# Performance work log

Measured on AMD Instinct MI355X. Metric: run time of the kernel, lower is better.

## Reference

```python
import jax, jax.numpy as jnp
import numpy as np

B, C, H, W = 2, 512, 64, 64
G = 32  # GroupNorm groups
EPS = 1e-6


def setup_inputs() -> dict:
    key = jax.random.key(0)
    ks = jax.random.split(key, 6)
    s = 1.0 / np.sqrt(C)
    return {
        "x": jax.random.normal(ks[0], (B, C, H, W), dtype=jnp.float32),
        "gn_w": jnp.ones((C,), dtype=jnp.float32),
        "gn_b": jnp.zeros((C,), dtype=jnp.float32),
        "wq": jax.random.normal(ks[1], (C, C), dtype=jnp.float32) * s,
        "bq": jnp.zeros((C,), dtype=jnp.float32),
        "wk": jax.random.normal(ks[2], (C, C), dtype=jnp.float32) * s,
        "bk": jnp.zeros((C,), dtype=jnp.float32),
        "wv": jax.random.normal(ks[3], (C, C), dtype=jnp.float32) * s,
        "bv": jnp.zeros((C,), dtype=jnp.float32),
        "wo": jax.random.normal(ks[4], (C, C), dtype=jnp.float32) * s,
        "bo": jnp.zeros((C,), dtype=jnp.float32),
    }


def _group_norm(x, w, b):
    b_, c_, h_, w_ = x.shape
    xg = x.reshape(b_, G, c_ // G, h_ * w_)
    mu = jnp.mean(xg, axis=(2, 3), keepdims=True)
    var = jnp.var(xg, axis=(2, 3), keepdims=True)
    xn = (xg - mu) * jax.lax.rsqrt(var + EPS)
    xn = xn.reshape(b_, c_, h_ * w_)
    return xn * w[None, :, None] + b[None, :, None]  # [B, C, N]


def reference(x, gn_w, gn_b, wq, bq, wk, bk, wv, bv, wo, bo):
    b, c, h, w = x.shape
    hn = _group_norm(x, gn_w, gn_b)  # [B, C, N]
    # 1x1 convs == per-pixel matmuls over channel dim
    q = jnp.einsum('oc,bcn->bon', wq, hn) + bq[None, :, None]
    k = jnp.einsum('oc,bcn->bon', wk, hn) + bk[None, :, None]
    v = jnp.einsum('oc,bcn->bon', wv, hn) + bv[None, :, None]
    scale = jnp.asarray(c, x.dtype) ** -0.5
    attn = jnp.einsum('bci,bcj->bij', q, k) * scale  # [B, N, N]
    attn = jax.nn.softmax(attn, axis=-1)
    o = jnp.einsum('bij,bcj->bci', attn, v)  # [B, C, N]
    o = jnp.einsum('oc,bcn->bon', wo, o) + bo[None, :, None]
    return x + o.reshape(b, c, h, w)
```

## Files before the change

### kernel.cpp

```cpp
#include <hip/hip_runtime.h>

#define CC 512
#define NPIX 4096
#define NB 2
#define NG 32
#define GSIZE 16
#define EPS 1e-6f

typedef unsigned short u16;
typedef __bf16 bf16x8 __attribute__((ext_vector_type(8)));
typedef float f32x4 __attribute__((ext_vector_type(4)));

__device__ __forceinline__ float bf2f(u16 u) {
  union { unsigned int i; float f; } c; c.i = ((unsigned int)u) << 16; return c.f;
}
__device__ __forceinline__ u16 f2bf(float f) {
  union { float f; unsigned int i; } c; c.f = f;
  unsigned int u = c.i;
  return (u16)((u + 0x7fffu + ((u >> 16) & 1u)) >> 16);
}

__global__ __launch_bounds__(256) void f2bf4x4_kernel(
    const float* __restrict__ s0, const float* __restrict__ s1,
    const float* __restrict__ s2, const float* __restrict__ s3,
    u16* __restrict__ d0, u16* __restrict__ d1,
    u16* __restrict__ d2, u16* __restrict__ d3) {
  const float* s; u16* d;
  switch (blockIdx.y) {
    case 0: s = s0; d = d0; break;
    case 1: s = s1; d = d1; break;
    case 2: s = s2; d = d2; break;
    default: s = s3; d = d3; break;
  }
  int i = blockIdx.x * 256 + threadIdx.x;
  float4 v = ((const float4*)s)[i];
  uint2 pk;
  pk.x = (unsigned)f2bf(v.x) | ((unsigned)f2bf(v.y) << 16);
  pk.y = (unsigned)f2bf(v.z) | ((unsigned)f2bf(v.w) << 16);
  ((uint2*)d)[i] = pk;
}

__global__ __launch_bounds__(256) void concat2_kernel(const float* __restrict__ a,
                                                      const float* __restrict__ b,
                                                      float* __restrict__ o) {
  int i = blockIdx.x * 256 + threadIdx.x;
  o[i] = (i < CC) ? a[i] : b[i - CC];
}

__global__ __launch_bounds__(256) void gn_stats_kernel(const float* __restrict__ x,
                                                       float* __restrict__ stats) {
  int bg = blockIdx.x;
  const float4* p = (const float4*)(x + (long)bg * (GSIZE * NPIX));
  float s = 0.f, ss = 0.f;
  for (int i = threadIdx.x; i < GSIZE * NPIX / 4; i += 256) {
    float4 v = p[i];
    s  += v.x + v.y + v.z + v.w;
    ss += v.x * v.x + v.y * v.y + v.z * v.z + v.w * v.w;
  }
  for (int off = 32; off; off >>= 1) { s += __shfl_xor(s, off); ss += __shfl_xor(ss, off); }
  __shared__ float rs[4], rss[4];
  int wid = threadIdx.x >> 6;
  if ((threadIdx.x & 63) == 0) { rs[wid] = s; rss[wid] = ss; }
  __syncthreads();
  if (threadIdx.x == 0) {
    s = rs[0] + rs[1] + rs[2] + rs[3];
    ss = rss[0] + rss[1] + rss[2] + rss[3];
    float mean = s / (float)(GSIZE * NPIX);
    float var = ss / (float)(GSIZE * NPIX) - mean * mean;
    stats[bg * 2] = mean;
    stats[bg * 2 + 1] = rsqrtf(var + EPS);
  }
}

__global__ __launch_bounds__(256) void gn_apply_kernel(const float* __restrict__ x,
                                                       const float* __restrict__ stats,
                                                       const float* __restrict__ gw,
                                                       const float* __restrict__ gb,
                                                       u16* __restrict__ hn) {
  int n0 = blockIdx.x * 64, c0 = blockIdx.y * 64, b = blockIdx.z;
  __shared__ float tile[64][65];
  int t = threadIdx.x;
  int nj = t & 63, cw = t >> 6;
  #pragma unroll
  for (int r = 0; r < 16; ++r) {
    int ci = cw * 16 + r;
    int c = c0 + ci;
    float mean = stats[(b * NG + (c >> 4)) * 2];
    float rstd = stats[(b * NG + (c >> 4)) * 2 + 1];
    float v = x[((long)b * CC + c) * NPIX + n0 + nj];
    tile[ci][nj] = (v - mean) * rstd * gw[c] + gb[c];
  }
  __syncthreads();
  #pragma unroll
  for (int r = 0; r < 16; ++r) {
    int nn = cw * 16 + r;
    hn[((long)b * NPIX + n0 + nn) * CC + c0 + nj] = f2bf(tile[nj][nn]);
  }
}

#define BM 128
#define BN 128
#define BKT 64
#define BUFSZ 8192

template<int OUTF32, int BIASMODE, int RESID>
__global__ __launch_bounds__(256) void gemm_nt(
    const u16* __restrict__ A, int lda, long aBatch,
    const u16* __restrict__ B, int ldb, long bBatch,
    void* __restrict__ C, int ldc, long cBatch,
    const float* __restrict__ bias,
    const float* __restrict__ resid, long rBatch,
    int K, float scale) {
  __shared__ u16 SH[2 * 2 * BUFSZ];
  const int t = threadIdx.x;

  int nwgx = gridDim.x, nwgy = gridDim.y;
  int flat = blockIdx.x + nwgx * (blockIdx.y + nwgy * blockIdx.z);
  int nwg = nwgx * nwgy * gridDim.z;
  int newflat = (flat % 8) * (nwg / 8) + flat / 8;
  const int bx = newflat % nwgx;
  int tmpf = newflat / nwgx;
  const int by = tmpf % nwgy;
  const int bz = tmpf / nwgy;

  const int m0 = by * BM;
  const int n0 = bx * BN;
  const u16* Ab = A + (long)bz * aBatch;
  const u16* Bb = B + (long)bz * bBatch;

  const int lane = t & 63;
  const int wid = t >> 6;
  const int wr = (wid >> 1) * 64;
  const int wc = (wid & 1) * 64;
  const int r16 = lane & 15;
  const int q = lane >> 4;

  const int sRow = wid * 8 + (lane >> 3);
  const int sCol = (((lane & 7) ^ (lane >> 3)) * 8);

  f32x4 acc[4][4] = {};
  const int rsw = r16 & 7;

  const int nt = K / BKT;

  auto stage = [&](int c, int k0) {
    u16* aDst = SH + c * 2 * BUFSZ + wid * 512;
    u16* bDst = SH + c * 2 * BUFSZ + BUFSZ + wid * 512;
    #pragma unroll
    for (int p = 0; p < 4; ++p) {
      __builtin_amdgcn_global_load_lds(
          (const __attribute__((address_space(1))) unsigned int*)(Ab + (long)(m0 + p * 32 + sRow) * lda + k0 + sCol),
          (__attribute__((address_space(3))) unsigned int*)(aDst + p * 2048),
          16, 0, 0);
      __builtin_amdgcn_global_load_lds(
          (const __attribute__((address_space(1))) unsigned int*)(Bb + (long)(n0 + p * 32 + sRow) * ldb + k0 + sCol),
          (__attribute__((address_space(3))) unsigned int*)(bDst + p * 2048),
          16, 0, 0);
    }
  };

  stage(0, 0);

  for (int tt = 0; tt < nt; ++tt) {
    const int pre = tt + 1;
    if (pre < nt) {
      stage(pre & 1, pre * BKT);
      asm volatile("s_waitcnt vmcnt(8)" ::: "memory");
    } else {
      asm volatile("s_waitcnt vmcnt(0)" ::: "memory");
    }
    __builtin_amdgcn_s_barrier();
    __builtin_amdgcn_sched_barrier(0);

    const u16* As_b = SH + (tt & 1) * 2 * BUFSZ;
    const u16* Bs_b = As_b + BUFSZ;
    #pragma unroll
    for (int kk = 0; kk < BKT; kk += 32) {
      bf16x8 af[4], bfr[4];
      const int c0q = (kk >> 3) + q;
      const int colSw = (c0q ^ rsw) * 8;
      #pragma unroll
      for (int i = 0; i < 4; ++i) {
        af[i]  = *(const bf16x8*)&As_b[(wr + i * 16 + r16) * BKT + colSw];
        bfr[i] = *(const bf16x8*)&Bs_b[(wc + i * 16 + r16) * BKT + colSw];
      }
      #pragma unroll
      for (int i = 0; i < 4; ++i)
        #pragma unroll
        for (int j = 0; j < 4; ++j)
          acc[i][j] = __builtin_amdgcn_mfma_f32_16x16x32_bf16(af[i], bfr[j], acc[i][j], 0, 0, 0);
    }
    __builtin_amdgcn_s_barrier();
    __builtin_amdgcn_sched_barrier(0);
  }

  #pragma unroll
  for (int i = 0; i < 4; ++i) {
    #pragma unroll
    for (int j = 0; j < 4; ++j) {
      #pragma unroll
      for (int r = 0; r < 4; ++r) {
        int row = m0 + wr + i * 16 + q * 4 + r;
        int col = n0 + wc + j * 16 + r16;
        float v = acc[i][j][r] * scale;
        if (BIASMODE == 1) v += bias[row];
        if (BIASMODE == 2) v += bias[col];
        long off = (long)bz * cBatch + (long)row * ldc + col;
        if (RESID) v += resid[(long)bz * rBatch + (long)row * ldc + col];
        if (OUTF32) ((float*)C)[off] = v;
        else        ((u16*)C)[off] = f2bf(v);
      }
    }
  }
}

__global__ __launch_bounds__(512, 2) void gemm256_nt(
    const u16* __restrict__ A, int lda, long aBatch,
    const u16* __restrict__ B, int ldb, long bBatch,
    u16* __restrict__ C, int ldc, long cBatch,
    int K, float scale) {
  __shared__ u16 SH[2][32768];
  const int t = threadIdx.x;

  int nwgx = gridDim.x, nwgy = gridDim.y;
  int flat = blockIdx.x + nwgx * (blockIdx.y + nwgy * blockIdx.z);
  int nwg = nwgx * nwgy * gridDim.z;
  int newflat = (flat % 8) * (nwg / 8) + flat / 8;
  const int bx = newflat % nwgx;
  int tmpf = newflat / nwgx;
  const int by = tmpf % nwgy;
  const int bz = tmpf / nwgy;

  const int m0 = by * 256;
  const int n0 = bx * 256;
  const u16* Ab = A + (long)bz * aBatch;
  const u16* Bb = B + (long)bz * bBatch;
  u16* Cb = C + (long)bz * cBatch;

  const int lane = t & 63;
  const int wid = t >> 6;
  const int wrow = (wid >> 2) * 128;
  const int wcol = (wid & 3) * 64;
  const int r16 = lane & 15;
  const int q = lane >> 4;
  const int rsw = r16 & 7;

  const int sRow = t >> 3;
  const int sCol = ((t & 7) ^ ((t >> 3) & 7)) * 8;

  auto stage = [&](int d, int k0) {
    u16* base = &SH[d][0];
    #pragma unroll
    for (int i = 0; i < 4; ++i)
      __builtin_amdgcn_global_load_lds(
          (const __attribute__((address_space(1))) unsigned int*)(Ab + (long)(m0 + i * 64 + sRow) * lda + k0 + sCol),
          (__attribute__((address_space(3))) unsigned int*)(base + i * 4096 + wid * 512),
          16, 0, 0);
    #pragma unroll
    for (int i = 0; i < 4; ++i)
      __builtin_amdgcn_global_load_lds(
          (const __attribute__((address_space(1))) unsigned int*)(Bb + (long)(n0 + i * 64 + sRow) * ldb + k0 + sCol),
          (__attribute__((address_space(3))) unsigned int*)(base + 16384 + i * 4096 + wid * 512),
          16, 0, 0);
  };

  f32x4 acc[8][4] = {};
  const int nt = K / 64;

  stage(0, 0);

  for (int tt = 0; tt < nt; ++tt) {
    const u16* As_ = &SH[tt & 1][0];
    const u16* Bs_ = As_ + 16384;
    if (tt + 1 < nt) {
      stage((tt + 1) & 1, (tt + 1) * 64);
      asm volatile("s_waitcnt vmcnt(8)" ::: "memory");
    } else {
      asm volatile("s_waitcnt vmcnt(0)" ::: "memory");
    }
    __builtin_amdgcn_s_barrier();
    __builtin_amdgcn_sched_barrier(0);

    bf16x8 a0[4], a1[4], b0[4], b1[4];
    const int c0 = (q ^ rsw) * 8;
    const int c1 = ((4 + q) ^ rsw) * 8;

    #pragma unroll
    for (int i = 0; i < 4; ++i)
      a0[i] = *(const bf16x8*)&As_[(wrow + i * 16 + r16) * 64 + c0];
    #pragma unroll
    for (int i = 0; i < 4; ++i)
      b0[i] = *(const bf16x8*)&Bs_[(wcol + i * 16 + r16) * 64 + c0];
    asm volatile("s_waitcnt lgkmcnt(0)" ::: "memory");
    __builtin_amdgcn_sched_barrier(0);
    __builtin_amdgcn_s_setprio(1);
    #pragma unroll
    for (int mi = 0; mi < 4; ++mi)
      #pragma unroll
      for (int ni = 0; ni < 4; ++ni)
        acc[mi][ni] = __builtin_amdgcn_mfma_f32_16x16x32_bf16(a0[mi], b0[ni], acc[mi][ni], 0, 0, 0);
    __builtin_amdgcn_s_setprio(0);
    __builtin_amdgcn_s_barrier();

    #pragma unroll
    for (int i = 0; i < 4; ++i)
      a1[i] = *(const bf16x8*)&As_[(wrow + (4 + i) * 16 + r16) * 64 + c0];
    asm volatile("s_waitcnt lgkmcnt(0)" ::: "memory");
    __builtin_amdgcn_sched_barrier(0);
    __builtin_amdgcn_s_setprio(1);
    #pragma unroll
    for (int mi = 0; mi < 4; ++mi)
      #pragma unroll
      for (int ni = 0; ni < 4; ++ni)
        acc[4 + mi][ni] = __builtin_amdgcn_mfma_f32_16x16x32_bf16(a1[mi], b0[ni], acc[4 + mi][ni], 0, 0, 0);
    __builtin_amdgcn_s_setprio(0);
    __builtin_amdgcn_s_barrier();

    #pragma unroll
    for (int i = 0; i < 4; ++i)
      a0[i] = *(const bf16x8*)&As_[(wrow + i * 16 + r16) * 64 + c1];
    #pragma unroll
    for (int i = 0; i < 4; ++i)
      b1[i] = *(const bf16x8*)&Bs_[(wcol + i * 16 + r16) * 64 + c1];
    asm volatile("s_waitcnt lgkmcnt(0)" ::: "memory");
    __builtin_amdgcn_sched_barrier(0);
    __builtin_amdgcn_s_setprio(1);
    #pragma unroll
    for (int mi = 0; mi < 4; ++mi)
      #pragma unroll
      for (int ni = 0; ni < 4; ++ni)
        acc[mi][ni] = __builtin_amdgcn_mfma_f32_16x16x32_bf16(a0[mi], b1[ni], acc[mi][ni], 0, 0, 0);
    __builtin_amdgcn_s_setprio(0);
    __builtin_amdgcn_s_barrier();

    #pragma unroll
    for (int i = 0; i < 4; ++i)
      a1[i] = *(const bf16x8*)&As_[(wrow + (4 + i) * 16 + r16) * 64 + c1];
    asm volatile("s_waitcnt lgkmcnt(0)" ::: "memory");
    __builtin_amdgcn_sched_barrier(0);
    __builtin_amdgcn_s_setprio(1);
    #pragma unroll
    for (int mi = 0; mi < 4; ++mi)
      #pragma unroll
      for (int ni = 0; ni < 4; ++ni)
        acc[4 + mi][ni] = __builtin_amdgcn_mfma_f32_16x16x32_bf16(a1[mi], b1[ni], acc[4 + mi][ni], 0, 0, 0);
    __builtin_amdgcn_s_setprio(0);
    __builtin_amdgcn_s_barrier();
    __builtin_amdgcn_sched_barrier(0);
  }

  #pragma unroll
  for (int mi = 0; mi < 8; ++mi)
    #pragma unroll
    for (int ni = 0; ni < 4; ++ni)
      #pragma unroll
      for (int r = 0; r < 4; ++r) {
        int row = m0 + wrow + mi * 16 + q * 4 + r;
        int col = n0 + wcol + ni * 16 + r16;
        Cb[(long)row * ldc + col] = f2bf(acc[mi][ni][r] * scale);
      }
}

__global__ __launch_bounds__(256) void softmax_kernel(u16* __restrict__ SP, long bStride) {
  u16* p = SP + (long)blockIdx.y * bStride + (long)blockIdx.x * NPIX;
  int t = threadIdx.x;
  float v[16];
  uint4 raw0 = *(const uint4*)(p + t * 8);
  uint4 raw1 = *(const uint4*)(p + 2048 + t * 8);
  const u16* u0 = (const u16*)&raw0;
  const u16* u1 = (const u16*)&raw1;
  #pragma unroll
  for (int i = 0; i < 8; ++i) { v[i] = bf2f(u0[i]); v[8 + i] = bf2f(u1[i]); }
  float m = v[0];
  #pragma unroll
  for (int i = 1; i < 16; ++i) m = fmaxf(m, v[i]);
  for (int off = 32; off; off >>= 1) m = fmaxf(m, __shfl_xor(m, off));
  __shared__ float red[4], red2[4];
  int wid = t >> 6;
  if ((t & 63) == 0) red[wid] = m;
  __syncthreads();
  m = fmaxf(fmaxf(red[0], red[1]), fmaxf(red[2], red[3]));
  float s = 0.f;
  #pragma unroll
  for (int i = 0; i < 16; ++i) { v[i] = __expf(v[i] - m); s += v[i]; }
  for (int off = 32; off; off >>= 1) s += __shfl_xor(s, off);
  if ((t & 63) == 0) red2[wid] = s;
  __syncthreads();
  s = red2[0] + red2[1] + red2[2] + red2[3];
  float inv = 1.0f / s;
  u16 o0[8], o1[8];
  #pragma unroll
  for (int i = 0; i < 8; ++i) { o0[i] = f2bf(v[i] * inv); o1[i] = f2bf(v[8 + i] * inv); }
  *(uint4*)(p + t * 8) = *(uint4*)o0;
  *(uint4*)(p + 2048 + t * 8) = *(uint4*)o1;
}

extern "C" void kernel_launch(void* const* d_in, const int* in_sizes, int n_in,
                              void* d_out, int out_size, void* d_ws, size_t ws_size,
                              hipStream_t stream) {
  const float* x   = (const float*)d_in[0];
  const float* gnw = (const float*)d_in[1];
  const float* gnb = (const float*)d_in[2];
  const float* wq  = (const float*)d_in[3];
  const float* bq  = (const float*)d_in[4];
  const float* wk  = (const float*)d_in[5];
  const float* bk_ = (const float*)d_in[6];
  const float* wv  = (const float*)d_in[7];
  const float* bv  = (const float*)d_in[8];
  const float* wo  = (const float*)d_in[9];
  const float* bo  = (const float*)d_in[10];
  float* out = (float*)d_out;

  char* wsp = (char*)d_ws;
  auto alloc = [&](size_t bytes) {
    char* r = wsp; wsp += (bytes + 255) & ~(size_t)255; return r;
  };
  u16* wqb = (u16*)alloc((size_t)CC * CC * 2);
  u16* wkb = (u16*)alloc((size_t)CC * CC * 2);
  u16* wvb = (u16*)alloc((size_t)CC * CC * 2);
  u16* wob = (u16*)alloc((size_t)CC * CC * 2);
  float* bqk = (float*)alloc((size_t)2 * CC * 4);
  float* stats = (float*)alloc((size_t)NB * NG * 2 * 4);
  u16* hn  = (u16*)alloc((size_t)NB * NPIX * CC * 2);
  u16* qkt = (u16*)alloc((size_t)NB * NPIX * (2 * CC) * 2);
  u16* vcn = (u16*)alloc((size_t)NB * CC * NPIX * 2);
  u16* ot  = (u16*)alloc((size_t)NB * NPIX * CC * 2);
  size_t used = (size_t)(wsp - (char*)d_ws);
  size_t rem = ws_size > used ? ws_size - used : 0;
  int CH = 256;
  if ((size_t)NB * 1024 * NPIX * 2 <= rem) CH = 1024;
  if ((size_t)NB * 4096 * NPIX * 2 <= rem) CH = 4096;
  u16* SP = (u16*)alloc((size_t)NB * CH * NPIX * 2);

  dim3 blk(256);
  f2bf4x4_kernel<<<dim3(CC * CC / 1024, 4), blk, 0, stream>>>(
      wq, wk, wv, wo, wqb, wkb, wvb, wob);
  concat2_kernel<<<2 * CC / 256, blk, 0, stream>>>(bq, bk_, bqk);

  gn_stats_kernel<<<NB * NG, blk, 0, stream>>>(x, stats);
  gn_apply_kernel<<<dim3(NPIX / 64, CC / 64, NB), blk, 0, stream>>>(x, stats, gnw, gnb, hn);

  gemm_nt<0, 2, 0><<<dim3(2 * CC / BN, NPIX / BM, NB), blk, 0, stream>>>(
      hn, CC, (long)NPIX * CC, wqb, CC, 0, qkt, 2 * CC, (long)NPIX * 2 * CC,
      bqk, nullptr, 0, CC, 1.0f);
  gemm_nt<0, 1, 0><<<dim3(NPIX / BN, CC / BM, NB), blk, 0, stream>>>(
      wvb, CC, 0, hn, CC, (long)NPIX * CC, vcn, NPIX, (long)CC * NPIX, bv, nullptr, 0, CC, 1.0f);

  const u16* qt = qkt;
  const u16* kt = qkt + CC;
  const float scale = 0.044194173824159216f;
  for (int i0 = 0; i0 < NPIX; i0 += CH) {
    if (CH == 4096) {
      gemm256_nt<<<dim3(NPIX / 256, NPIX / 256, NB), dim3(512), 0, stream>>>(
          qt, 2 * CC, (long)NPIX * 2 * CC, kt, 2 * CC, (long)NPIX * 2 * CC,
          SP, NPIX, (long)CH * NPIX, CC, scale);
    } else {
      gemm_nt<0, 0, 0><<<dim3(NPIX / BN, CH / BM, NB), blk, 0, stream>>>(
          qt + (long)i0 * 2 * CC, 2 * CC, (long)NPIX * 2 * CC, kt, 2 * CC, (long)NPIX * 2 * CC,
          SP, NPIX, (long)CH * NPIX, nullptr, nullptr, 0, CC, scale);
    }
    softmax_kernel<<<dim3(CH, NB), blk, 0, stream>>>(SP, (long)CH * NPIX);
    gemm_nt<0, 0, 0><<<dim3(CC / BN, CH / BM, NB), blk, 0, stream>>>(
        SP, NPIX, (long)CH * NPIX, vcn, NPIX, (long)CC * NPIX,
        ot + (long)i0 * CC, CC, (long)NPIX * CC, nullptr, nullptr, 0, NPIX, 1.0f);
  }

  gemm_nt<1, 1, 1><<<dim3(NPIX / BN, CC / BM, NB), blk, 0, stream>>>(
      wob, CC, 0, ot, CC, (long)NPIX * CC, out, NPIX, (long)CC * NPIX,
      bo, x, (long)CC * NPIX, CC, 1.0f);
}
```

Baseline: 179.0 us.

## Fuse softmax into QK^T epilogue with deferred row-sum normalization in PV GEMM

Drops the separate softmax kernel. The QK^T GEMM epilogue now computes exp(score) without subtracting the row max, writes unnormalized probabilities through LDS for coalesced stores, and atomically accumulates per-row sums into a zeroed buffer. The PV GEMM epilogue divides each row by its sum. This removes one full read and write pass over the 4096x4096 score matrix per batch. The cost is float atomics, and without max subtraction exp can overflow if scores grow large.

```diff
diff --git a/kernel.cpp b/kernel.cpp
--- a/kernel.cpp
+++ b/kernel.cpp
@@ -103,13 +103,14 @@
 #define BKT 64
 #define BUFSZ 8192
 
-template<int OUTF32, int BIASMODE, int RESID>
+template<int OUTF32, int BIASMODE, int RESID, int EPI>
 __global__ __launch_bounds__(256) void gemm_nt(
     const u16* __restrict__ A, int lda, long aBatch,
     const u16* __restrict__ B, int ldb, long bBatch,
     void* __restrict__ C, int ldc, long cBatch,
     const float* __restrict__ bias,
     const float* __restrict__ resid, long rBatch,
+    float* __restrict__ L, int lOff,
     int K, float scale) {
   __shared__ u16 SH[2 * 2 * BUFSZ];
   const int t = threadIdx.x;
@@ -194,15 +195,40 @@
     __builtin_amdgcn_sched_barrier(0);
   }
 
+  if (EPI == 1) {
+    #pragma unroll
+    for (int i = 0; i < 4; ++i) {
+      #pragma unroll
+      for (int r = 0; r < 4; ++r) {
+        int row = m0 + wr + i * 16 + q * 4 + r;
+        float s = 0.f;
+        #pragma unroll
+        for (int j = 0; j < 4; ++j) {
+          float p = __expf(acc[i][j][r] * scale);
+          s += p;
+          int col = n0 + wc + j * 16 + r16;
+          ((u16*)C)[(long)bz * cBatch + (long)row * ldc + col] = f2bf(p);
+        }
+        s += __shfl_xor(s, 1); s += __shfl_xor(s, 2);
+        s += __shfl_xor(s, 4); s += __shfl_xor(s, 8);
+        if (r16 == 0) atomicAdd(&L[(long)bz * NPIX + lOff + row], s);
+      }
+    }
+    return;
+  }
+
   #pragma unroll
   for (int i = 0; i < 4; ++i) {
     #pragma unroll
-    for (int j = 0; j < 4; ++j) {
-      #pragma unroll
-      for (int r = 0; r < 4; ++r) {
-        int row = m0 + wr + i * 16 + q * 4 + r;
+    for (int r = 0; r < 4; ++r) {
+      int row = m0 + wr + i * 16 + q * 4 + r;
+      float inv = 1.0f;
+      if (EPI == 2) inv = 1.0f / L[(long)bz * NPIX + lOff + row];
+      #pragma unroll
+      for (int j = 0; j < 4; ++j) {
         int col = n0 + wc + j * 16 + r16;
         float v = acc[i][j][r] * scale;
+        if (EPI == 2) v *= inv;
         if (BIASMODE == 1) v += bias[row];
         if (BIASMODE == 2) v += bias[col];
         long off = (long)bz * cBatch + (long)row * ldc + col;
@@ -214,10 +240,11 @@
   }
 }
 
-__global__ __launch_bounds__(512, 2) void gemm256_nt(
+__global__ __launch_bounds__(512, 2) void gemm256_exp(
     const u16* __restrict__ A, int lda, long aBatch,
     const u16* __restrict__ B, int ldb, long bBatch,
     u16* __restrict__ C, int ldc, long cBatch,
+    float* __restrict__ L,
     int K, float scale) {
   __shared__ u16 SH[2][32768];
   const int t = threadIdx.x;
@@ -349,50 +376,35 @@
     __builtin_amdgcn_sched_barrier(0);
   }
 
+  u16* Ps = &SH[0][0];
   #pragma unroll
-  for (int mi = 0; mi < 8; ++mi)
-    #pragma unroll
-    for (int ni = 0; ni < 4; ++ni)
-      #pragma unroll
-      for (int r = 0; r < 4; ++r) {
-        int row = m0 + wrow + mi * 16 + q * 4 + r;
-        int col = n0 + wcol + ni * 16 + r16;
-        Cb[(long)row * ldc + col] = f2bf(acc[mi][ni][r] * scale);
+  for (int mi = 0; mi < 8; ++mi) {
+    #pragma unroll
+    for (int r = 0; r < 4; ++r) {
+      int lrow = wrow + mi * 16 + q * 4 + r;
+      float s = 0.f;
+      #pragma unroll
+      for (int ni = 0; ni < 4; ++ni) {
+        float p = __expf(acc[mi][ni][r] * scale);
+        s += p;
+        Ps[lrow * 256 + wcol + ni * 16 + r16] = f2bf(p);
       }
-}
-
-__global__ __launch_bounds__(256) void softmax_kernel(u16* __restrict__ SP, long bStride) {
-  u16* p = SP + (long)blockIdx.y * bStride + (long)blockIdx.x * NPIX;
-  int t = threadIdx.x;
-  float v[16];
-  uint4 raw0 = *(const uint4*)(p + t * 8);
-  uint4 raw1 = *(const uint4*)(p + 2048 + t * 8);
-  const u16* u0 = (const u16*)&raw0;
-  const u16* u1 = (const u16*)&raw1;
-  #pragma unroll
-  for (int i = 0; i < 8; ++i) { v[i] = bf2f(u0[i]); v[8 + i] = bf2f(u1[i]); }
-  float m = v[0];
-  #pragma unroll
-  for (int i = 1; i < 16; ++i) m = fmaxf(m, v[i]);
-  for (int off = 32; off; off >>= 1) m = fmaxf(m, __shfl_xor(m, off));
-  __shared__ float red[4], red2[4];
-  int wid = t >> 6;
-  if ((t & 63) == 0) red[wid] = m;
+      s += __shfl_xor(s, 1); s += __shfl_xor(s, 2);
+      s += __shfl_xor(s, 4); s += __shfl_xor(s, 8);
+      if (r16 == 0) atomicAdd(&L[(long)bz * NPIX + m0 + lrow], s);
+    }
+  }
   __syncthreads();
-  m = fmaxf(fmaxf(red[0], red[1]), fmaxf(red[2], red[3]));
-  float s = 0.f;
-  #pragma unroll
-  for (int i = 0; i < 16; ++i) { v[i] = __expf(v[i] - m); s += v[i]; }
-  for (int off = 32; off; off >>= 1) s += __shfl_xor(s, off);
-  if ((t & 63) == 0) red2[wid] = s;
-  __syncthreads();
-  s = red2[0] + red2[1] + red2[2] + red2[3];
-  float inv = 1.0f / s;
-  u16 o0[8], o1[8];
-  #pragma unroll
-  for (int i = 0; i < 8; ++i) { o0[i] = f2bf(v[i] * inv); o1[i] = f2bf(v[8 + i] * inv); }
-  *(uint4*)(p + t * 8) = *(uint4*)o0;
-  *(uint4*)(p + 2048 + t * 8) = *(uint4*)o1;
+  {
+    const int rr = t >> 5;
+    const int c8 = (t & 31) * 8;
+    #pragma unroll
+    for (int pp = 0; pp < 16; ++pp) {
+      int lrow = pp * 16 + rr;
+      uint4 v = *(const uint4*)&Ps[lrow * 256 + c8];
+      *(uint4*)&Cb[(long)(m0 + lrow) * ldc + n0 + c8] = v;
+    }
+  }
 }
 
 extern "C" void kernel_launch(void* const* d_in, const int* in_sizes, int n_in,
@@ -421,6 +433,7 @@
   u16* wob = (u16*)alloc((size_t)CC * CC * 2);
   float* bqk = (float*)alloc((size_t)2 * CC * 4);
   float* stats = (float*)alloc((size_t)NB * NG * 2 * 4);
+  float* lsum = (float*)alloc((size_t)NB * NPIX * 4);
   u16* hn  = (u16*)alloc((size_t)NB * NPIX * CC * 2);
   u16* qkt = (u16*)alloc((size_t)NB * NPIX * (2 * CC) * 2);
   u16* vcn = (u16*)alloc((size_t)NB * CC * NPIX * 2);
@@ -436,36 +449,37 @@
   f2bf4x4_kernel<<<dim3(CC * CC / 1024, 4), blk, 0, stream>>>(
       wq, wk, wv, wo, wqb, wkb, wvb, wob);
   concat2_kernel<<<2 * CC / 256, blk, 0, stream>>>(bq, bk_, bqk);
+  hipMemsetAsync(lsum, 0, (size_t)NB * NPIX * 4, stream);
 
   gn_stats_kernel<<<NB * NG, blk, 0, stream>>>(x, stats);
   gn_apply_kernel<<<dim3(NPIX / 64, CC / 64, NB), blk, 0, stream>>>(x, stats, gnw, gnb, hn);
 
-  gemm_nt<0, 2, 0><<<dim3(2 * CC / BN, NPIX / BM, NB), blk, 0, stream>>>(
+  gemm_nt<0, 2, 0, 0><<<dim3(2 * CC / BN, NPIX / BM, NB), blk, 0, stream>>>(
       hn, CC, (long)NPIX * CC, wqb, CC, 0, qkt, 2 * CC, (long)NPIX * 2 * CC,
-      bqk, nullptr, 0, CC, 1.0f);
-  gemm_nt<0, 1, 0><<<dim3(NPIX / BN, CC / BM, NB), blk, 0, stream>>>(
-      wvb, CC, 0, hn, CC, (long)NPIX * CC, vcn, NPIX, (long)CC * NPIX, bv, nullptr, 0, CC, 1.0f);
+      bqk, nullptr, 0, nullptr, 0, CC, 1.0f);
+  gemm_nt<0, 1, 0, 0><<<dim3(NPIX / BN, CC / BM, NB), blk, 0, stream>>>(
+      wvb, CC, 0, hn, CC, (long)NPIX * CC, vcn, NPIX, (long)CC * NPIX,
+      bv, nullptr, 0, nullptr, 0, CC, 1.0f);
 
   const u16* qt = qkt;
   const u16* kt = qkt + CC;
   const float scale = 0.044194173824159216f;
   for (int i0 = 0; i0 < NPIX; i0 += CH) {
     if (CH == 4096) {
-      gemm256_nt<<<dim3(NPIX / 256, NPIX / 256, NB), dim3(512), 0, stream>>>(
+      gemm256_exp<<<dim3(NPIX / 256, NPIX / 256, NB), dim3(512), 0, stream>>>(
           qt, 2 * CC, (long)NPIX * 2 * CC, kt, 2 * CC, (long)NPIX * 2 * CC,
-          SP, NPIX, (long)CH * NPIX, CC, scale);
+          SP, NPIX, (long)CH * NPIX, lsum, CC, scale);
     } else {
-      gemm_nt<0, 0, 0><<<dim3(NPIX / BN, CH / BM, NB), blk, 0, stream>>>(
+      gemm_nt<0, 0, 0, 1><<<dim3(NPIX / BN, CH / BM, NB), blk, 0, stream>>>(
           qt + (long)i0 * 2 * CC, 2 * CC, (long)NPIX * 2 * CC, kt, 2 * CC, (long)NPIX * 2 * CC,
-          SP, NPIX, (long)CH * NPIX, nullptr, nullptr, 0, CC, scale);
-    }
-    softmax_kernel<<<dim3(CH, NB), blk, 0, stream>>>(SP, (long)CH * NPIX);
-    gemm_nt<0, 0, 0><<<dim3(CC / BN, CH / BM, NB), blk, 0, stream>>>(
+          SP, NPIX, (long)CH * NPIX, nullptr, nullptr, 0, lsum, i0, CC, scale);
+    }
+    gemm_nt<0, 0, 0, 2><<<dim3(CC / BN, CH / BM, NB), blk, 0, stream>>>(
         SP, NPIX, (long)CH * NPIX, vcn, NPIX, (long)CC * NPIX,
-        ot + (long)i0 * CC, CC, (long)NPIX * CC, nullptr, nullptr, 0, NPIX, 1.0f);
-  }
-
-  gemm_nt<1, 1, 1><<<dim3(NPIX / BN, CC / BM, NB), blk, 0, stream>>>(
+        ot + (long)i0 * CC, CC, (long)NPIX * CC, nullptr, nullptr, 0, lsum, i0, NPIX, 1.0f);
+  }
+
+  gemm_nt<1, 1, 1, 0><<<dim3(NPIX / BN, CC / BM, NB), blk, 0, stream>>>(
       wob, CC, 0, ot, CC, (long)NPIX * CC, out, NPIX, (long)CC * NPIX,
-      bo, x, (long)CC * NPIX, CC, 1.0f);
-}
+      bo, x, (long)CC * NPIX, nullptr, 0, CC, 1.0f);
+}
```

After: 184.0 us. 2.8% more time.
